# Performance work log

Measured on AMD Instinct MI355X. Metric: run time of the kernel, lower is better.

The kernel has to match this reference:

```python
import jax, jax.numpy as jnp
import numpy as np

MAX_SPAN_LENGTH = 4


def setup_inputs() -> dict:
    key = jax.random.key(0)
    ks = jax.random.split(key, 6)
    B, S, H, E = 8, 2048, 768, 32
    hidden_states = jax.random.normal(ks[0], (B, S, H), jnp.float32)
    topic_vector = jax.random.normal(ks[1], (B, H), jnp.float32)
    text_mask = jnp.ones((B, S), dtype=bool)
    length_embedding = jax.random.normal(ks[2], (MAX_SPAN_LENGTH + 1, E), jnp.float32) * 0.02
    W1 = jax.random.normal(ks[3], (3 * H + E, H), jnp.float32) * 0.02
    b1 = jnp.zeros((H,), jnp.float32)
    W2 = jax.random.normal(ks[4], (H, 1), jnp.float32) * 0.02
    b2 = jnp.zeros((1,), jnp.float32)
    return {"hidden_states": hidden_states, "topic_vector": topic_vector,
            "text_mask": text_mask, "length_embedding": length_embedding,
            "W1": W1, "b1": b1, "W2": W2, "b2": b2}


def reference(hidden_states, topic_vector, text_mask, length_embedding, W1, b1, W2, b2):
    B, S, H = hidden_states.shape
    L = MAX_SPAN_LENGTH
    NEG = jnp.float32(-jnp.inf)

    # Static span grid (text_mask is full): span k = (start, start+off), off in [0, L)
    offs = jnp.arange(L)
    starts = jnp.repeat(jnp.arange(S), L)          # [N] with N = S*L
    ends = starts + jnp.tile(offs, S)              # [N]
    valid = ends < S                               # pad spans running off the end
    ends_c = jnp.minimum(ends, S - 1)
    lengths = jnp.tile(offs + 1, S)                # [N] in [1, L]

    start_v = hidden_states[:, starts, :]          # [B,N,H] gather span starts
    end_v = hidden_states[:, ends_c, :]            # [B,N,H] gather span ends
    len_v = length_embedding[lengths]              # [N,E]
    N = starts.shape[0]
    topic = jnp.broadcast_to(topic_vector[:, None, :], (B, N, H))
    feats = jnp.concatenate(
        [topic, start_v, end_v, jnp.broadcast_to(len_v[None], (B, N, len_v.shape[-1]))],
        axis=-1)                                   # [B,N,3H+E]

    h = jax.nn.gelu(feats @ W1 + b1, approximate=False)   # [B,N,H]
    span_scores = (h @ W2)[..., 0] + b2[0]                 # [B,N]
    span_scores = jnp.where(valid[None, :], span_scores, NEG)

    # Project span scores back to tokens via masked max over covering spans
    tok = jnp.arange(S)
    cover = (tok[None, :] >= starts[:, None]) & (tok[None, :] <= ends_c[:, None])  # [N,S]
    token_scores = jnp.max(
        jnp.where(cover[None, :, :], span_scores[:, :, None], NEG), axis=1)       # [B,S]
    token_scores = jnp.where(text_mask, token_scores, NEG)
    return token_scores, span_scores
```

## Files before the change

kernel.cpp:

```cpp
#include <hip/hip_runtime.h>
#include <math.h>

#define B 8
#define S 2048
#define H 768
#define E 32
#define L 4
#define M (B*S)
#define NCOL (2*H)
#define K 768

#define NEG_SENTINEL (-1.0e30f)

typedef float v4f __attribute__((ext_vector_type(4)));
typedef short v8s __attribute__((ext_vector_type(8)));
typedef _Float16 v8h __attribute__((ext_vector_type(8)));
typedef _Float16 v4h __attribute__((ext_vector_type(4)));

__device__ __forceinline__ int cperm_true(int cp) {
  return (cp & ~63) | (((cp & 3) << 4) | ((cp >> 2) & 15));
}

__device__ __forceinline__ void bfsplit(float f, unsigned short& h, unsigned short& l) {
  unsigned u = __float_as_uint(f);
  unsigned r = u + 0x7FFF + ((u >> 16) & 1);
  h = (unsigned short)(r >> 16);
  float fh = __uint_as_float(r & 0xFFFF0000u);
  float fl = f - fh;
  unsigned u2 = __float_as_uint(fl);
  unsigned r2 = u2 + 0x7FFF + ((u2 >> 16) & 1);
  l = (unsigned short)(r2 >> 16);
}
__device__ __forceinline__ void split4(float4 f, uint2& h, uint2& l) {
  unsigned short h0,h1,h2,h3,l0,l1,l2,l3;
  bfsplit(f.x,h0,l0); bfsplit(f.y,h1,l1); bfsplit(f.z,h2,l2); bfsplit(f.w,h3,l3);
  h.x = (unsigned)h0 | ((unsigned)h1 << 16); h.y = (unsigned)h2 | ((unsigned)h3 << 16);
  l.x = (unsigned)l0 | ((unsigned)l1 << 16); l.y = (unsigned)l2 | ((unsigned)l3 << 16);
}

__device__ __forceinline__ float gelu_f(float x) {
  float y  = x * 0.70710678118654752f;
  float ay = fabsf(y);
  float t  = __builtin_amdgcn_rcpf(fmaf(0.3275911f, ay, 1.0f));
  float poly = t * fmaf(t, fmaf(t, fmaf(t, fmaf(t, 1.061405429f, -1.453152027f),
                                        1.421413741f), -0.284496736f), 0.254829592f);
  float e  = __expf(-y * y);
  float er = 1.0f - poly * e;
  er = __builtin_copysignf(er, y);
  return 0.5f * x * (1.0f + er);
}


#define SPLITA_BLOCKS 1024
#define CONVW_BLOCKS 288
#define MISC_BLOCKS 39
#define TOPICW_BLOCKS 768

__global__ __launch_bounds__(256) void prep(
    const float* __restrict__ A, const float* __restrict__ W1,
    const float* __restrict__ lenemb, const float* __restrict__ b1,
    const float* __restrict__ W2,
    _Float16* __restrict__ Af, _Float16* __restrict__ Wf,
    float* __restrict__ topicW, float* __restrict__ lenbase,
    float* __restrict__ W2p)
{
  __shared__ __align__(16) char pshm[16 * 776 * 2];
  int bx = blockIdx.x;
  if (bx < SPLITA_BLOCKS) {
    _Float16* sl = (_Float16*)pshm;
    const float4* Ab = (const float4*)(A + (size_t)bx * 16 * K);
    #pragma unroll
    for (int rnd = 0; rnd < 12; rnd++) {
      int o4 = rnd * 256 + threadIdx.x;
      float4 fv = Ab[o4];
      int r = o4 / 192;
      int c = (o4 - r * 192) * 4;
      v4h hv;
      hv[0] = (_Float16)fv.x; hv[1] = (_Float16)fv.y;
      hv[2] = (_Float16)fv.z; hv[3] = (_Float16)fv.w;
      *(v4h*)(&sl[r * 776 + c]) = hv;
    }
    __syncthreads();
    _Float16* dst = Af + (size_t)bx * 12288;
    #pragma unroll
    for (int rnd = 0; rnd < 6; rnd++) {
      int cc = rnd * 256 + threadIdx.x;
      int r = cc & 15, kc = cc >> 4;
      v8h hv = *(v8h*)(&sl[r * 776 + kc * 8]);
      *(v8h*)(dst + (size_t)cc * 8) = hv;
    }
  } else if (bx < SPLITA_BLOCKS + CONVW_BLOCKS) {
    float (*t)[65] = (float(*)[65])pshm;
    int blk = bx - SPLITA_BLOCKS;
    int kb = blk % (K / 64);
    int nb = blk / (K / 64);
    int k0 = kb * 64, n0 = nb * 64;
    int tn = threadIdx.x & 63, tk = threadIdx.x >> 6;
    int n = n0 + tn;
    const float* src = (n < H) ? (W1 + (size_t)(H + k0) * H + n)
                               : (W1 + (size_t)(2 * H + k0) * H + (n - H));
    #pragma unroll
    for (int s = 0; s < 16; s++) {
      int kk = tk + s * 4;
      t[kk][tn] = src[(size_t)kk * H];
    }
    __syncthreads();
    int tkk = threadIdx.x & 63, tnn = threadIdx.x >> 6;
    #pragma unroll
    for (int s = 0; s < 16; s++) {
      int nn = tnn + s * 4;
      float v = t[tkk][nn];
      int n_g = n0 + nn;
      int kk_g = k0 + tkk;
      size_t go = ((size_t)((n_g >> 4) * 96 + (kk_g >> 3)) * 16 + (n_g & 15)) * 8
                + (kk_g & 7);
      Wf[go] = (_Float16)v;
    }
  } else {
    int idx = (bx - SPLITA_BLOCKS - CONVW_BLOCKS) * 256 + threadIdx.x;
    if (idx < L * H) {
      int l = idx / H, cp = idx % H;
      int h = cperm_true(cp);
      float s = b1[h];
      const float* le = lenemb + (size_t)(l + 1) * E;
      #pragma unroll
      for (int e = 0; e < E; e++)
        s = fmaf(le[e], W1[(size_t)(3 * H + e) * H + h], s);
      lenbase[idx] = s;
    } else if (idx < L * H + B * H) {
      topicW[idx - L * H] = 0.f;
    } else if (idx < L * H + B * H + H) {
      int cp = idx - L * H - B * H;
      W2p[cp] = W2[cperm_true(cp)];
    }
  }
}

__global__ __launch_bounds__(256, 2) void gemm_mfma(
    const _Float16* __restrict__ Af, const _Float16* __restrict__ Wf,
    const float* __restrict__ topic, const float* __restrict__ W1,
    float* __restrict__ topicW,
    _Float16* __restrict__ P, _Float16* __restrict__ Q)
{
  __shared__ float red[4][64];
  int tid = threadIdx.x, lane = tid & 63, wv = tid >> 6;
  int f = blockIdx.x;

  if (f >= (M / 128) * (NCOL / 128)) {
    int tw = f - (M / 128) * (NCOL / 128);
    int b = tw / 96;
    int r = tw % 96;
    int h0 = (r / 8) * 64;
    int kc0 = (r % 8) * 96;
    int hcol = tid & 63, ksub = tid >> 6;
    const float* tp = topic + (size_t)b * H;
    float s = 0.f;
    #pragma unroll
    for (int i = 0; i < 24; i++) {
      int k = kc0 + ksub * 24 + i;
      s = fmaf(tp[k], W1[(size_t)k * H + h0 + hcol], s);
    }
    red[ksub][hcol] = s;
    __syncthreads();
    if (tid < 64) {
      int cpo = ((tid & 15) << 2) | (tid >> 4);
      float tot = red[0][tid] + red[1][tid] + red[2][tid] + red[3][tid];
      atomicAdd(&topicW[(size_t)b * H + h0 + cpo], tot);
    }
    return;
  }

  int xcd = f & 7, g = f >> 3;
  int mb = xcd * 16 + (g / 12);
  int nb = g % 12;
  int wm = (wv >> 1) * 64, wn = (wv & 1) * 64;
  int kg = lane >> 4, fr = lane & 15;

  int aoff[4], boff[4];
  #pragma unroll
  for (int i = 0; i < 4; i++) {
    aoff[i] = ((mb * 8 + (wm >> 4) + i) * 96) * 128 + lane * 8;
    boff[i] = ((nb * 8 + (wn >> 4) + i) * 96) * 128 + lane * 8;
  }

  v4f acc[4][4];
  #pragma unroll
  for (int i = 0; i < 4; i++)
    #pragma unroll
    for (int j = 0; j < 4; j++) { v4f z = {0.f,0.f,0.f,0.f}; acc[i][j] = z; }

  v8h a[3][4], b[3][4];

  #define LOADF(BUF, IT)                                                       \
    { int ko = (IT) * 512;                                                     \
      _Pragma("unroll")                                                        \
      for (int i = 0; i < 4; i++) {                                            \
        a[BUF][i] = *(const v8h*)(Af + aoff[i] + ko);                          \
        b[BUF][i] = *(const v8h*)(Wf + boff[i] + ko);                          \
      } }

  #define COMPUTE(BUF)                                                         \
    { __builtin_amdgcn_s_setprio(1);                                           \
      _Pragma("unroll")                                                        \
      for (int j = 0; j < 4; j++)                                              \
        _Pragma("unroll")                                                      \
        for (int i = 0; i < 4; i++)                                            \
          acc[i][j] = __builtin_amdgcn_mfma_f32_16x16x32_f16(                  \
              a[BUF][i], b[BUF][j], acc[i][j], 0, 0, 0);                       \
      __builtin_amdgcn_s_setprio(0); }

  LOADF(0, 0);
  LOADF(1, 1);
  #pragma unroll
  for (int o = 0; o < 8; o++) {
    int i2 = (3 * o + 2) % 24;
    int i3 = (3 * o + 3) % 24;
    int i4 = (3 * o + 4) % 24;
    LOADF(2, i2);
    COMPUTE(0);
    LOADF(0, i3);
    COMPUTE(1);
    LOADF(1, i4);
    COMPUTE(2);
  }
  #undef LOADF
  #undef COMPUTE

  int m0 = mb * 128, n0 = nb * 128;
  _Float16* outB = (nb < 6) ? P : Q;
  int cb = (nb < 6) ? n0 : (n0 - H);
  int cbase = cb + wn + fr * 4;
  #pragma unroll
  for (int i = 0; i < 4; i++) {
    int row0 = m0 + wm + i * 16 + kg * 4;
    #pragma unroll
    for (int r = 0; r < 4; r++) {
      v4h pk;
      pk[0] = (_Float16)acc[i][0][r];
      pk[1] = (_Float16)acc[i][1][r];
      pk[2] = (_Float16)acc[i][2][r];
      pk[3] = (_Float16)acc[i][3][r];
      *(v4h*)(outB + (size_t)(row0 + r) * H + cbase) = pk;
    }
  }
}


__global__ __launch_bounds__(192) void combine(
    const _Float16* __restrict__ P, const _Float16* __restrict__ Q,
    const float* __restrict__ topicW, const float* __restrict__ lenbase,
    const float* __restrict__ W2p, const float* __restrict__ b2,
    float* __restrict__ spanOut)
{
  __shared__ float part[3][16];
  int tid = threadIdx.x, lane = tid & 63, wv = tid >> 6;
  int gs0 = blockIdx.x * 4;
  int b = gs0 >> 11;
  int s0 = gs0 & (S - 1);
  int gmax = (b + 1) * S - 1;
  int co = 4 * lane + 256 * wv;

  float4 w2 = *(const float4*)(W2p + co);
  float4 tv = *(const float4*)(topicW + (size_t)b * H + co);
  float4 bv[4];
  #pragma unroll
  for (int l = 0; l < L; l++) {
    float4 lv = *(const float4*)(lenbase + (size_t)l * H + co);
    bv[l].x = tv.x + lv.x; bv[l].y = tv.y + lv.y;
    bv[l].z = tv.z + lv.z; bv[l].w = tv.w + lv.w;
  }
  float4 p[4], q[7];
  #pragma unroll
  for (int si = 0; si < 4; si++) {
    v4h ph = *(const v4h*)(P + (size_t)(gs0 + si) * H + co);
    p[si].x = (float)ph[0]; p[si].y = (float)ph[1];
    p[si].z = (float)ph[2]; p[si].w = (float)ph[3];
  }
  #pragma unroll
  for (int r = 0; r < 7; r++) {
    int grow = gs0 + r; if (grow > gmax) grow = gmax;
    v4h qh = *(const v4h*)(Q + (size_t)grow * H + co);
    q[r].x = (float)qh[0]; q[r].y = (float)qh[1];
    q[r].z = (float)qh[2]; q[r].w = (float)qh[3];
  }

  float acc[4][4];
  #pragma unroll
  for (int si = 0; si < 4; si++) {
    #pragma unroll
    for (int l = 0; l < L; l++) {
      int r = si + l;
      float a0 = 0.f;
      a0 = fmaf(gelu_f(bv[l].x + p[si].x + q[r].x), w2.x, a0);
      a0 = fmaf(gelu_f(bv[l].y + p[si].y + q[r].y), w2.y, a0);
      a0 = fmaf(gelu_f(bv[l].z + p[si].z + q[r].z), w2.z, a0);
      a0 = fmaf(gelu_f(bv[l].w + p[si].w + q[r].w), w2.w, a0);
      acc[si][l] = a0;
    }
  }

  #pragma unroll
  for (int off = 32; off; off >>= 1)
    #pragma unroll
    for (int si = 0; si < 4; si++)
      #pragma unroll
      for (int l = 0; l < L; l++)
        acc[si][l] += __shfl_xor(acc[si][l], off, 64);

  if (lane == 0) {
    #pragma unroll
    for (int si = 0; si < 4; si++)
      #pragma unroll
      for (int l = 0; l < L; l++)
        part[wv][si * 4 + l] = acc[si][l];
  }
  __syncthreads();
  if (tid < 16) {
    int si = tid >> 2, l = tid & 3;
    float v = part[0][tid] + part[1][tid] + part[2][tid] + b2[0];
    int s = s0 + si;
    if (s + l >= S) v = NEG_SENTINEL;
    spanOut[(size_t)b * (S * L) + (size_t)s * L + l] = v;
  }
}

__global__ void token_max(const float* __restrict__ spanOut,
                          float* __restrict__ tokenOut)
{
  int idx = blockIdx.x * 256 + threadIdx.x;
  if (idx >= B * S) return;
  int b = idx >> 11, t = idx & (S - 1);
  float m = -INFINITY;
  int slo = max(t - (L - 1), 0);
  for (int sb = slo; sb <= t; sb++)
    for (int l = t - sb; l < L; l++)
      m = fmaxf(m, spanOut[(size_t)b * (S * L) + sb * L + l]);
  tokenOut[idx] = m;
}


__global__ __launch_bounds__(256) void conv_w_old(
    const float* __restrict__ W1,
    unsigned short* __restrict__ Wh, unsigned short* __restrict__ Wl)
{
  __shared__ float t[64][65];
  int kb = blockIdx.x % (K / 64);
  int nb = blockIdx.x / (K / 64);
  int k0 = kb * 64, n0 = nb * 64;
  int tn = threadIdx.x & 63, tk = threadIdx.x >> 6;
  int n = n0 + tn;
  const float* src = (n < H) ? (W1 + (size_t)(H + k0) * H + n)
                             : (W1 + (size_t)(2 * H + k0) * H + (n - H));
  #pragma unroll
  for (int s = 0; s < 16; s++) {
    int kk = tk + s * 4;
    t[kk][tn] = src[(size_t)kk * H];
  }
  __syncthreads();
  int tkk = threadIdx.x & 63, tnn = threadIdx.x >> 6;
  #pragma unroll
  for (int s = 0; s < 16; s++) {
    int nn = tnn + s * 4;
    float v = t[tkk][nn];
    unsigned short hi, lo;
    bfsplit(v, hi, lo);
    size_t go = (size_t)(n0 + nn) * K + k0 + tkk;
    Wh[go] = hi; Wl[go] = lo;
  }
}

__global__ __launch_bounds__(256) void gemm_old(
    const float* __restrict__ A,
    const unsigned short* __restrict__ Wh,
    const unsigned short* __restrict__ Wl,
    float* __restrict__ P, float* __restrict__ Q)
{
  __shared__ __align__(16) unsigned short Ah_t[128 * 32];
  __shared__ __align__(16) unsigned short Al_t[128 * 32];
  __shared__ __align__(16) unsigned short Bh_t[128 * 32];
  __shared__ __align__(16) unsigned short Bl_t[128 * 32];

  int tid = threadIdx.x;
  int lane = tid & 63, wv = tid >> 6;
  int n0 = blockIdx.x * 128;
  int m0 = blockIdx.y * 128;
  int sr = tid >> 1;
  int sc = (tid & 1) * 16;
  const float* Ap = A + (size_t)(m0 + sr) * K + sc;
  const unsigned short* Bph = Wh + (size_t)(n0 + sr) * K + sc;
  const unsigned short* Bpl = Wl + (size_t)(n0 + sr) * K + sc;
  int wm = (wv >> 1) * 64;
  int wn = (wv & 1) * 64;
  int kg = lane >> 4;
  int fr = lane & 15;

  v4f acc[4][4];
  #pragma unroll
  for (int i = 0; i < 4; i++)
    #pragma unroll
    for (int j = 0; j < 4; j++) { v4f z = {0.f,0.f,0.f,0.f}; acc[i][j] = z; }

  for (int k0 = 0; k0 < K; k0 += 32) {
    float4 a0 = *(const float4*)(Ap + k0);
    float4 a1 = *(const float4*)(Ap + k0 + 4);
    float4 a2 = *(const float4*)(Ap + k0 + 8);
    float4 a3 = *(const float4*)(Ap + k0 + 12);
    uint4 bh0 = *(const uint4*)(Bph + k0);
    uint4 bh1 = *(const uint4*)(Bph + k0 + 8);
    uint4 bl0 = *(const uint4*)(Bpl + k0);
    uint4 bl1 = *(const uint4*)(Bpl + k0 + 8);
    __syncthreads();
    uint2 h0,h1,h2,h3, l0,l1,l2,l3;
    split4(a0,h0,l0); split4(a1,h1,l1); split4(a2,h2,l2); split4(a3,h3,l3);
    uint4 H0 = {h0.x,h0.y,h1.x,h1.y}, H1 = {h2.x,h2.y,h3.x,h3.y};
    uint4 L0 = {l0.x,l0.y,l1.x,l1.y}, L1 = {l2.x,l2.y,l3.x,l3.y};
    *(uint4*)&Ah_t[sr*32 + sc]     = H0;
    *(uint4*)&Ah_t[sr*32 + sc + 8] = H1;
    *(uint4*)&Al_t[sr*32 + sc]     = L0;
    *(uint4*)&Al_t[sr*32 + sc + 8] = L1;
    *(uint4*)&Bh_t[sr*32 + sc]     = bh0;
    *(uint4*)&Bh_t[sr*32 + sc + 8] = bh1;
    *(uint4*)&Bl_t[sr*32 + sc]     = bl0;
    *(uint4*)&Bl_t[sr*32 + sc + 8] = bl1;
    __syncthreads();
    v8s ah[4], al[4], bh[4], bl[4];
    #pragma unroll
    for (int i = 0; i < 4; i++) {
      ah[i] = *(v8s*)&Ah_t[(wm + i*16 + fr)*32 + kg*8];
      al[i] = *(v8s*)&Al_t[(wm + i*16 + fr)*32 + kg*8];
      bh[i] = *(v8s*)&Bh_t[(wn + i*16 + fr)*32 + kg*8];
      bl[i] = *(v8s*)&Bl_t[(wn + i*16 + fr)*32 + kg*8];
    }
    #pragma unroll
    for (int i = 0; i < 4; i++)
      #pragma unroll
      for (int j = 0; j < 4; j++) {
        acc[i][j] = __builtin_amdgcn_mfma_f32_16x16x32_bf16(ah[i], bh[j], acc[i][j], 0, 0, 0);
        acc[i][j] = __builtin_amdgcn_mfma_f32_16x16x32_bf16(ah[i], bl[j], acc[i][j], 0, 0, 0);
        acc[i][j] = __builtin_amdgcn_mfma_f32_16x16x32_bf16(al[i], bh[j], acc[i][j], 0, 0, 0);
      }
  }
  float* outB = (n0 < H) ? P : Q;
  int cb = (n0 < H) ? n0 : (n0 - H);
  #pragma unroll
  for (int i = 0; i < 4; i++) {
    int row0 = m0 + wm + i*16 + kg*4;
    #pragma unroll
    for (int j = 0; j < 4; j++) {
      int col = cb + wn + j*16 + fr;
      #pragma unroll
      for (int r = 0; r < 4; r++)
        outB[(size_t)(row0 + r) * H + col] = acc[i][j][r];
    }
  }
}

__global__ void compute_base(const float* __restrict__ topic,
                             const float* __restrict__ lenemb,
                             const float* __restrict__ W1,
                             const float* __restrict__ b1,
                             float* __restrict__ base)
{
  int idx = blockIdx.x * 256 + threadIdx.x;
  if (idx >= B * L * H) return;
  int h = idx % H;
  int bl = idx / H;
  int l = bl % L;
  int b = bl / L;
  float sacc = b1[h];
  const float* t = topic + b * H;
  for (int k = 0; k < H; k++)
    sacc = fmaf(t[k], W1[(size_t)k * H + h], sacc);
  const float* le = lenemb + (l + 1) * E;
  for (int e = 0; e < E; e++)
    sacc = fmaf(le[e], W1[(size_t)(3 * H + e) * H + h], sacc);
  base[idx] = sacc;
}

__global__ __launch_bounds__(256) void combine_f32(
    const float* __restrict__ P, const float* __restrict__ Q,
    const float* __restrict__ base,
    const float* __restrict__ W2, const float* __restrict__ b2,
    float* __restrict__ spanOut)
{
  int tid = threadIdx.x, lane = tid & 63, wv = tid >> 6;
  int siteBase = blockIdx.x * 16;
  int b = siteBase >> 11;
  int c0 = 4 * lane;
  float4 w2v[3], bv[4][3];
  #pragma unroll
  for (int j = 0; j < 3; j++) {
    w2v[j] = *(const float4*)(W2 + c0 + 256 * j);
    #pragma unroll
    for (int l = 0; l < L; l++)
      bv[l][j] = *(const float4*)(base + ((size_t)(b * L + l)) * H + c0 + 256 * j);
  }
  float bb2 = b2[0];

  #pragma unroll
  for (int si = 0; si < 4; si++) {
    int site = siteBase + wv * 4 + si;
    int s = site & (S - 1);
    const float* Prow = P + (size_t)site * H;
    float4 p[3];
    #pragma unroll
    for (int j = 0; j < 3; j++) p[j] = *(const float4*)(Prow + c0 + 256 * j);
    float acc[4];
    #pragma unroll
    for (int l = 0; l < L; l++) {
      int e = min(s + l, S - 1);
      const float* Qrow = Q + ((size_t)(b * S + e)) * H;
      float a = 0.f;
      #pragma unroll
      for (int j = 0; j < 3; j++) {
        float4 q = *(const float4*)(Qrow + c0 + 256 * j);
        a = fmaf(gelu_f(bv[l][j].x + p[j].x + q.x), w2v[j].x, a);
        a = fmaf(gelu_f(bv[l][j].y + p[j].y + q.y), w2v[j].y, a);
        a = fmaf(gelu_f(bv[l][j].z + p[j].z + q.z), w2v[j].z, a);
        a = fmaf(gelu_f(bv[l][j].w + p[j].w + q.w), w2v[j].w, a);
      }
      acc[l] = a;
    }
    #pragma unroll
    for (int off = 32; off; off >>= 1)
      #pragma unroll
      for (int l = 0; l < L; l++) acc[l] += __shfl_xor(acc[l], off, 64);
    if (lane == 0) {
      #pragma unroll
      for (int l = 0; l < L; l++) {
        float v = (s + l < S) ? (acc[l] + bb2) : NEG_SENTINEL;
        spanOut[(size_t)b * (S * L) + s * L + l] = v;
      }
    }
  }
}

extern "C" void kernel_launch(void* const* d_in, const int* in_sizes, int n_in,
                              void* d_out, int out_size, void* d_ws, size_t ws_size,
                              hipStream_t stream) {
  const float* hidden = (const float*)d_in[0];
  const float* topic  = (const float*)d_in[1];
  const float* lenemb = (const float*)d_in[3];
  const float* W1     = (const float*)d_in[4];
  const float* b1     = (const float*)d_in[5];
  const float* W2     = (const float*)d_in[6];
  const float* b2     = (const float*)d_in[7];

  float* out = (float*)d_out;
  float* tokenOut = out;
  float* spanOut  = out + B * S;

  size_t need = (size_t)(2 * M * H + M * K + NCOL * K) * 2
              + (size_t)(B * H + L * H + H) * 4;

  if (ws_size >= need) {
    _Float16* Pm = (_Float16*)d_ws;
    _Float16* Qm = Pm + (size_t)M * H;
    _Float16* Af = Qm + (size_t)M * H;
    _Float16* Wf = Af + (size_t)M * K;
    float* topicW  = (float*)(Wf + (size_t)NCOL * K);
    float* lenbase = topicW + (size_t)B * H;
    float* W2p     = lenbase + (size_t)L * H;

    prep<<<SPLITA_BLOCKS + CONVW_BLOCKS + MISC_BLOCKS, 256, 0, stream>>>(
        hidden, W1, lenemb, b1, W2, Af, Wf, topicW, lenbase, W2p);
    gemm_mfma<<<(M / 128) * (NCOL / 128) + TOPICW_BLOCKS, 256, 0, stream>>>(
        Af, Wf, topic, W1, topicW, Pm, Qm);
    combine<<<M / 4, 192, 0, stream>>>(Pm, Qm, topicW, lenbase, W2p, b2, spanOut);
    token_max<<<(B * S + 255) / 256, 256, 0, stream>>>(spanOut, tokenOut);
  } else {
    float* Pm = (float*)d_ws;
    float* Qm = Pm + (size_t)M * H;
    unsigned short* Wh = (unsigned short*)(Qm + (size_t)M * H);
    unsigned short* Wl = Wh + (size_t)NCOL * K;
    float* base = (float*)(Wl + (size_t)NCOL * K);

    conv_w_old<<<(K / 64) * (NCOL / 64), 256, 0, stream>>>(W1, Wh, Wl);
    compute_base<<<(B * L * H + 255) / 256, 256, 0, stream>>>(topic, lenemb, W1, b1, base);
    gemm_old<<<dim3(NCOL / 128, M / 128), 256, 0, stream>>>(hidden, Wh, Wl, Pm, Qm);
    combine_f32<<<(B * S) / 16, 256, 0, stream>>>(Pm, Qm, base, W2, b2, spanOut);
    token_max<<<(B * S + 255) / 256, 256, 0, stream>>>(spanOut, tokenOut);
  }
}
```

Before: 177.8 us.

## Give each wave its own span sites in combine, removing cross-wave reduction

```diff
diff --git a/kernel.cpp b/kernel.cpp
--- a/kernel.cpp
+++ b/kernel.cpp
@@ -246,56 +246,87 @@
 }
 
 
-__global__ __launch_bounds__(192) void combine(
+__global__ __launch_bounds__(256) void combine(
     const _Float16* __restrict__ P, const _Float16* __restrict__ Q,
     const float* __restrict__ topicW, const float* __restrict__ lenbase,
     const float* __restrict__ W2p, const float* __restrict__ b2,
     float* __restrict__ spanOut)
 {
-  __shared__ float part[3][16];
   int tid = threadIdx.x, lane = tid & 63, wv = tid >> 6;
-  int gs0 = blockIdx.x * 4;
-  int b = gs0 >> 11;
+  int siteBase = blockIdx.x * 16;
+  int b = siteBase >> 11;
+  int gs0 = siteBase + wv * 4;
   int s0 = gs0 & (S - 1);
   int gmax = (b + 1) * S - 1;
-  int co = 4 * lane + 256 * wv;
-
-  float4 w2 = *(const float4*)(W2p + co);
-  float4 tv = *(const float4*)(topicW + (size_t)b * H + co);
-  float4 bv[4];
-  #pragma unroll
-  for (int l = 0; l < L; l++) {
-    float4 lv = *(const float4*)(lenbase + (size_t)l * H + co);
-    bv[l].x = tv.x + lv.x; bv[l].y = tv.y + lv.y;
-    bv[l].z = tv.z + lv.z; bv[l].w = tv.w + lv.w;
-  }
-  float4 p[4], q[7];
-  #pragma unroll
-  for (int si = 0; si < 4; si++) {
-    v4h ph = *(const v4h*)(P + (size_t)(gs0 + si) * H + co);
-    p[si].x = (float)ph[0]; p[si].y = (float)ph[1];
-    p[si].z = (float)ph[2]; p[si].w = (float)ph[3];
-  }
+  int c0 = 4 * lane;
+  float bb2 = b2[0];
+
+  int qrow[7];
   #pragma unroll
   for (int r = 0; r < 7; r++) {
-    int grow = gs0 + r; if (grow > gmax) grow = gmax;
-    v4h qh = *(const v4h*)(Q + (size_t)grow * H + co);
-    q[r].x = (float)qh[0]; q[r].y = (float)qh[1];
-    q[r].z = (float)qh[2]; q[r].w = (float)qh[3];
-  }
+    int g = gs0 + r;
+    qrow[r] = (g > gmax) ? gmax : g;
+  }
+
+  v4h pb[2][4], qb[2][7];
+  #pragma unroll
+  for (int si = 0; si < 4; si++)
+    pb[0][si] = *(const v4h*)(P + (size_t)(gs0 + si) * H + c0);
+  #pragma unroll
+  for (int r = 0; r < 7; r++)
+    qb[0][r] = *(const v4h*)(Q + (size_t)qrow[r] * H + c0);
 
   float acc[4][4];
   #pragma unroll
-  for (int si = 0; si < 4; si++) {
+  for (int si = 0; si < 4; si++)
+    #pragma unroll
+    for (int l = 0; l < L; l++) acc[si][l] = 0.f;
+
+  #pragma unroll
+  for (int j = 0; j < 3; j++) {
+    const int cur = j & 1, nxt = cur ^ 1;
+    if (j < 2) {
+      int con = c0 + 256 * (j + 1);
+      #pragma unroll
+      for (int si = 0; si < 4; si++)
+        pb[nxt][si] = *(const v4h*)(P + (size_t)(gs0 + si) * H + con);
+      #pragma unroll
+      for (int r = 0; r < 7; r++)
+        qb[nxt][r] = *(const v4h*)(Q + (size_t)qrow[r] * H + con);
+    }
+    int co = c0 + 256 * j;
+    float4 w2 = *(const float4*)(W2p + co);
+    float4 tv = *(const float4*)(topicW + (size_t)b * H + co);
+    float4 bv[4];
     #pragma unroll
     for (int l = 0; l < L; l++) {
-      int r = si + l;
-      float a0 = 0.f;
-      a0 = fmaf(gelu_f(bv[l].x + p[si].x + q[r].x), w2.x, a0);
-      a0 = fmaf(gelu_f(bv[l].y + p[si].y + q[r].y), w2.y, a0);
-      a0 = fmaf(gelu_f(bv[l].z + p[si].z + q[r].z), w2.z, a0);
-      a0 = fmaf(gelu_f(bv[l].w + p[si].w + q[r].w), w2.w, a0);
-      acc[si][l] = a0;
+      float4 lv = *(const float4*)(lenbase + (size_t)l * H + co);
+      bv[l].x = tv.x + lv.x; bv[l].y = tv.y + lv.y;
+      bv[l].z = tv.z + lv.z; bv[l].w = tv.w + lv.w;
+    }
+    float4 p[4], q[7];
+    #pragma unroll
+    for (int si = 0; si < 4; si++) {
+      p[si].x = (float)pb[cur][si][0]; p[si].y = (float)pb[cur][si][1];
+      p[si].z = (float)pb[cur][si][2]; p[si].w = (float)pb[cur][si][3];
+    }
+    #pragma unroll
+    for (int r = 0; r < 7; r++) {
+      q[r].x = (float)qb[cur][r][0]; q[r].y = (float)qb[cur][r][1];
+      q[r].z = (float)qb[cur][r][2]; q[r].w = (float)qb[cur][r][3];
+    }
+    #pragma unroll
+    for (int si = 0; si < 4; si++) {
+      #pragma unroll
+      for (int l = 0; l < L; l++) {
+        int r = si + l;
+        float a0 = acc[si][l];
+        a0 = fmaf(gelu_f(bv[l].x + p[si].x + q[r].x), w2.x, a0);
+        a0 = fmaf(gelu_f(bv[l].y + p[si].y + q[r].y), w2.y, a0);
+        a0 = fmaf(gelu_f(bv[l].z + p[si].z + q[r].z), w2.z, a0);
+        a0 = fmaf(gelu_f(bv[l].w + p[si].w + q[r].w), w2.w, a0);
+        acc[si][l] = a0;
+      }
     }
   }
 
@@ -309,18 +340,14 @@
 
   if (lane == 0) {
     #pragma unroll
-    for (int si = 0; si < 4; si++)
-      #pragma unroll
-      for (int l = 0; l < L; l++)
-        part[wv][si * 4 + l] = acc[si][l];
-  }
-  __syncthreads();
-  if (tid < 16) {
-    int si = tid >> 2, l = tid & 3;
-    float v = part[0][tid] + part[1][tid] + part[2][tid] + b2[0];
-    int s = s0 + si;
-    if (s + l >= S) v = NEG_SENTINEL;
-    spanOut[(size_t)b * (S * L) + (size_t)s * L + l] = v;
+    for (int si = 0; si < 4; si++) {
+      int s = s0 + si;
+      #pragma unroll
+      for (int l = 0; l < L; l++) {
+        float v = (s + l < S) ? (acc[si][l] + bb2) : NEG_SENTINEL;
+        spanOut[(size_t)b * (S * L) + (size_t)s * L + l] = v;
+      }
+    }
   }
 }
 
@@ -566,7 +593,7 @@
         hidden, W1, lenemb, b1, W2, Af, Wf, topicW, lenbase, W2p);
     gemm_mfma<<<(M / 128) * (NCOL / 128) + TOPICW_BLOCKS, 256, 0, stream>>>(
         Af, Wf, topic, W1, topicW, Pm, Qm);
-    combine<<<M / 4, 192, 0, stream>>>(Pm, Qm, topicW, lenbase, W2p, b2, spanOut);
+    combine<<<(B * S) / 16, 256, 0, stream>>>(Pm, Qm, topicW, lenbase, W2p, b2, spanOut);
     token_max<<<(B * S + 255) / 256, 256, 0, stream>>>(spanOut, tokenOut);
   } else {
     float* Pm = (float*)d_ws;
```

Result: no change. 179.6 us (+1.0%).
